# Performance work log

Hardware: AMD Instinct MI355X
Metric: run time of the kernel (lower is better)

## Reference

```python
import jax, jax.numpy as jnp
import numpy as np

E, T, H, I, K = 8, 8192, 1024, 4096, 2  # experts, tokens, hidden, intermediate, top_k


def setup_inputs() -> dict:
    key = jax.random.key(0)
    k1, k2, k3, k4 = jax.random.split(key, 4)
    return {
        "hidden_states": jax.random.normal(k1, (T, H), dtype=jnp.float32),
        "router_weight": jax.random.normal(k2, (E, H), dtype=jnp.float32) * 0.02,
        "gate_up_proj": jax.random.normal(k3, (E, 2 * I, H), dtype=jnp.float32) * 0.02,
        "down_proj": jax.random.normal(k4, (E, H, I), dtype=jnp.float32) * 0.02,
    }


def reference(hidden_states, router_weight, gate_up_proj, down_proj):
    x = hidden_states  # [T, H]
    # --- TopKRouter ---
    router_logits = x @ router_weight.T  # [T, E]
    routing_probs = jax.nn.softmax(router_logits.astype(jnp.float32), axis=-1)
    top_k_weights, top_k_indices = jax.lax.top_k(routing_probs, K)  # [T, K]
    top_k_weights = top_k_weights / jnp.sum(top_k_weights, axis=-1, keepdims=True)  # norm_topk_prob
    top_k_weights = top_k_weights.astype(router_logits.dtype)
    # --- MoEExperts: dense combine weight per (token, expert) ---
    # w_dense[t, e] = sum_k top_k_weights[t, k] * (top_k_indices[t, k] == e)
    tok = jnp.arange(x.shape[0])[:, None]
    w_dense = jnp.zeros((x.shape[0], E), dtype=x.dtype).at[tok, top_k_indices].add(top_k_weights)
    out = jnp.zeros_like(x)
    for e in range(E):  # fixed small expert loop (structurally distinct weights)
        gu = x @ gate_up_proj[e].T          # [T, 2I]
        gate, up = jnp.split(gu, 2, axis=-1)
        y = (jax.nn.silu(gate) * up) @ down_proj[e].T  # [T, H]
        out = out + w_dense[:, e:e + 1] * y
    return out
```

## Files before the change

### kernel.cpp

```cpp
#include <hip/hip_runtime.h>
#include <stdint.h>
#include <math.h>

#define NE 8
#define NT 8192
#define NH 1024
#define NI 4096
#define BM 128
#define BK 32

typedef _Float16 half8 __attribute__((ext_vector_type(8)));
typedef float f32x4 __attribute__((ext_vector_type(4)));

#define OFF_X16   (512u << 10)
#define OFF_ACT   (18u << 20)
#define OFF_GUP16 (146ull << 20)
#define OFF_DP16  (274ull << 20)

__device__ __forceinline__ half8 pack_half8(float4 a, float4 b) {
  half8 h;
  h[0] = (_Float16)a.x; h[1] = (_Float16)a.y; h[2] = (_Float16)a.z; h[3] = (_Float16)a.w;
  h[4] = (_Float16)b.x; h[5] = (_Float16)b.y; h[6] = (_Float16)b.z; h[7] = (_Float16)b.w;
  return h;
}

__device__ __forceinline__ void gload16(const void* g, void* l) {
  __builtin_amdgcn_global_load_lds(
      (const __attribute__((address_space(1))) uint32_t*)g,
      (__attribute__((address_space(3))) uint32_t*)l, 16, 0, 0);
}

#define PIPE_WAIT(N) asm volatile("s_waitcnt vmcnt(" #N ")" ::: "memory")
#define PIPE_BAR() do { asm volatile("" ::: "memory"); \
                        __builtin_amdgcn_s_barrier(); \
                        asm volatile("" ::: "memory"); } while (0)

__global__ __launch_bounds__(256) void convert_w(
    const float* __restrict__ src, _Float16* __restrict__ dst, int n8)
{
  int stride = gridDim.x * 256;
  for (int i = blockIdx.x * 256 + threadIdx.x; i < n8; i += stride) {
    const float4* p = (const float4*)(src + (size_t)i * 8);
    float4 a = p[0], b = p[1];
    *(half8*)(dst + (size_t)i * 8) = pack_half8(a, b);
  }
}

__global__ __launch_bounds__(256) void moe_router(
    const float* __restrict__ x, const float* __restrict__ rw,
    int* __restrict__ iws, _Float16* __restrict__ x16)
{
  int wid  = threadIdx.x >> 6;
  int lane = threadIdx.x & 63;
  int t = (blockIdx.x << 2) + wid;

  const float4* xp4 = (const float4*)(x + (size_t)t * NH + lane * 16);
  float xv[16];
  #pragma unroll
  for (int j = 0; j < 4; ++j) {
    float4 v = xp4[j];
    xv[4*j+0] = v.x; xv[4*j+1] = v.y; xv[4*j+2] = v.z; xv[4*j+3] = v.w;
  }
  half8 h0, h1;
  #pragma unroll
  for (int j = 0; j < 8; ++j) { h0[j] = (_Float16)xv[j]; h1[j] = (_Float16)xv[8+j]; }
  half8* xo = (half8*)(x16 + (size_t)t * NH + lane * 16);
  xo[0] = h0; xo[1] = h1;

  float lg[NE];
  #pragma unroll
  for (int e = 0; e < NE; ++e) {
    const float4* wp4 = (const float4*)(rw + e * NH + lane * 16);
    float s = 0.f;
    #pragma unroll
    for (int j = 0; j < 4; ++j) {
      float4 w = wp4[j];
      s += xv[4*j+0]*w.x + xv[4*j+1]*w.y + xv[4*j+2]*w.z + xv[4*j+3]*w.w;
    }
    lg[e] = s;
  }
  #pragma unroll
  for (int d = 32; d > 0; d >>= 1) {
    #pragma unroll
    for (int e = 0; e < NE; ++e) lg[e] += __shfl_xor(lg[e], d, 64);
  }
  if (lane == 0) {
    int e0 = 0;
    #pragma unroll
    for (int e = 1; e < NE; ++e) if (lg[e] > lg[e0]) e0 = e;
    int e1 = (e0 == 0) ? 1 : 0;
    #pragma unroll
    for (int e = 0; e < NE; ++e) if (e != e0 && lg[e] > lg[e1]) e1 = e;
    float p1 = expf(lg[e1] - lg[e0]);
    float s  = 1.f + p1;
    int*   te = iws + 64;
    float* tw = (float*)(iws + 64 + NT*2);
    te[2*t]   = e0; te[2*t+1] = e1;
    tw[2*t]   = 1.f / s; tw[2*t+1] = p1 / s;
    atomicAdd(iws + e0, 1);
    atomicAdd(iws + e1, 1);
  }
}

__global__ void moe_scan(int* iws) {
  if (threadIdx.x == 0 && blockIdx.x == 0) {
    int* cnt = iws; int* off = iws + 8; int* mbc = iws + 25;
    int o = 0, m = 0;
    for (int e = 0; e < NE; ++e) {
      off[e] = o; mbc[e] = m;
      o += cnt[e]; m += (cnt[e] + BM - 1) / BM;
    }
    off[NE] = o; mbc[NE] = m;
  }
}

__global__ __launch_bounds__(256) void moe_fill(int* __restrict__ iws) {
  int t = blockIdx.x * 256 + threadIdx.x;
  const int*   te = iws + 64;
  const float* tw = (const float*)(iws + 64 + NT*2);
  int*   cursor   = iws + 17;
  const int* off  = iws + 8;
  int*   tok_slot = iws + 64 + NT*4;
  float* w_slot   = (float*)(iws + 64 + NT*6);
  #pragma unroll
  for (int k = 0; k < 2; ++k) {
    int e = te[2*t+k];
    int pos = atomicAdd(&cursor[e], 1);
    int s = off[e] + pos;
    tok_slot[s] = t;
    w_slot[s]   = tw[2*t+k];
  }
}


__global__ __launch_bounds__(256, 2) void moe_gemm1_f16(
    const _Float16* __restrict__ x16, const _Float16* __restrict__ gup16,
    const int* __restrict__ iws, _Float16* __restrict__ act)
{
  const int* cnt = iws; const int* off = iws + 8; const int* mbc = iws + 25;
  const int* tok_slot = iws + 64 + NT*4;
  int bid = blockIdx.x;
  int mb  = bid >> 6;
  int i0  = (bid & 63) << 6;
  if (mb >= mbc[NE]) return;
  int e = 0;
  while (mb >= mbc[e+1]) ++e;
  int mloc  = mb - mbc[e];
  int row0  = off[e] + mloc * BM;
  int nrows = cnt[e] - mloc * BM; if (nrows > BM) nrows = BM;

  __shared__ __align__(16) _Float16 Al [3][BM * BK];
  __shared__ __align__(16) _Float16 Bgl[3][64 * BK];
  __shared__ __align__(16) _Float16 Bul[3][64 * BK];

  int tid = threadIdx.x, wid = tid >> 6, lane = tid & 63;
  int sr0 = wid*16 + (lane >> 2);
  int sr1 = 64 + sr0;
  int slot = lane & 3;
  int ks0 = (slot ^ ((sr0 >> 1) & 3)) * 8;
  int ks1 = (slot ^ ((sr1 >> 1) & 3)) * 8;

  int tok0 = tok_slot[row0 + (sr0 < nrows ? sr0 : 0)];
  int tok1 = tok_slot[row0 + (sr1 < nrows ? sr1 : 0)];
  const _Float16* pA0 = x16 + (size_t)tok0 * NH + ks0;
  const _Float16* pA1 = x16 + (size_t)tok1 * NH + ks1;
  const _Float16* pBg = gup16 + ((size_t)e*2*NI + i0 + sr0) * NH + ks0;
  const _Float16* pBu = pBg + (size_t)NI * NH;

  int wr = (wid >> 1) * 64, wc = (wid & 1) * 32;
  int fr = lane & 15, fq = lane >> 4;

  f32x4 accG[4][2] = {};
  f32x4 accU[4][2] = {};

  _Float16 *A0 = &Al[0][0], *A1 = &Al[1][0], *A2 = &Al[2][0];
  _Float16 *G0 = &Bgl[0][0], *G1 = &Bgl[1][0], *G2 = &Bgl[2][0];
  _Float16 *U0 = &Bul[0][0], *U1 = &Bul[1][0], *U2 = &Bul[2][0];

#define STAGE1(Ab, Gb, Ub, kk) do { \
    gload16(pA0 + (kk), (Ab) + wid*512); \
    gload16(pA1 + (kk), (Ab) + (4+wid)*512); \
    gload16(pBg + (kk), (Gb) + wid*512); \
    gload16(pBu + (kk), (Ub) + wid*512); \
  } while (0)

#define COMPUTE1(Ab, Gb, Ub) do { \
    half8 aF[4]; \
    _Pragma("unroll") \
    for (int m = 0; m < 4; ++m) { \
      int r = wr + m*16 + fr; \
      aF[m] = *(const half8*)((Ab) + r*BK + ((fq ^ ((r>>1)&3)) * 8)); \
    } \
    __builtin_amdgcn_s_setprio(1); \
    _Pragma("unroll") \
    for (int n = 0; n < 2; ++n) { \
      int rb = wc + n*16 + fr; \
      int bo = rb*BK + ((fq ^ ((rb>>1)&3)) * 8); \
      half8 bg = *(const half8*)((Gb) + bo); \
      half8 bu = *(const half8*)((Ub) + bo); \
      _Pragma("unroll") \
      for (int m = 0; m < 4; ++m) \
        accG[m][n] = __builtin_amdgcn_mfma_f32_16x16x32_f16(aF[m], bg, accG[m][n], 0, 0, 0); \
      _Pragma("unroll") \
      for (int m = 0; m < 4; ++m) \
        accU[m][n] = __builtin_amdgcn_mfma_f32_16x16x32_f16(aF[m], bu, accU[m][n], 0, 0, 0); \
    } \
    __builtin_amdgcn_s_setprio(0); \
  } while (0)

#define ROT1() do { _Float16* t_; \
    t_ = A0; A0 = A1; A1 = A2; A2 = t_; \
    t_ = G0; G0 = G1; G1 = G2; G2 = t_; \
    t_ = U0; U0 = U1; U1 = U2; U2 = t_; } while (0)

  STAGE1(A0, G0, U0, 0);
  STAGE1(A1, G1, U1, BK);

  for (int k0 = 0; k0 + 2*BK < NH; k0 += BK) {
    PIPE_WAIT(4);
    PIPE_BAR();
    STAGE1(A2, G2, U2, k0 + 2*BK);
    COMPUTE1(A0, G0, U0);
    ROT1();
  }
  PIPE_WAIT(4);
  PIPE_BAR();
  COMPUTE1(A0, G0, U0);
  ROT1();
  PIPE_WAIT(0);
  PIPE_BAR();
  COMPUTE1(A0, G0, U0);

#undef STAGE1
#undef COMPUTE1
#undef ROT1

  #pragma unroll
  for (int m = 0; m < 4; ++m) {
    #pragma unroll
    for (int j = 0; j < 4; ++j) {
      int rl = wr + m*16 + fq*4 + j;
      if (rl < nrows) {
        _Float16* dst = act + (size_t)(row0 + rl) * NI + i0 + wc + fr;
        #pragma unroll
        for (int n = 0; n < 2; ++n) {
          float g = accG[m][n][j], u = accU[m][n][j];
          float a = (g / (1.f + __expf(-g))) * u;
          dst[n*16] = (_Float16)a;
        }
      }
    }
  }
}

__global__ __launch_bounds__(256, 4) void moe_gemm2_f16(
    const _Float16* __restrict__ act, const _Float16* __restrict__ dp16,
    const int* __restrict__ iws, float* __restrict__ out)
{
  const int* cnt = iws; const int* off = iws + 8; const int* mbc = iws + 25;
  const int* tok_slot = iws + 64 + NT*4;
  const float* w_slot = (const float*)(iws + 64 + NT*6);
  int bid = blockIdx.x;
  int mb  = bid >> 4;
  int h0  = (bid & 15) << 6;
  if (mb >= mbc[NE]) return;
  int e = 0;
  while (mb >= mbc[e+1]) ++e;
  int mloc  = mb - mbc[e];
  int row0  = off[e] + mloc * BM;
  int nrows = cnt[e] - mloc * BM; if (nrows > BM) nrows = BM;

  __shared__ __align__(16) _Float16 Al[3][BM * BK];
  __shared__ __align__(16) _Float16 Bl[3][64 * BK];

  int tid = threadIdx.x, wid = tid >> 6, lane = tid & 63;
  int sr0 = wid*16 + (lane >> 2);
  int sr1 = 64 + sr0;
  int slot = lane & 3;
  int ks0 = (slot ^ ((sr0 >> 1) & 3)) * 8;
  int ks1 = (slot ^ ((sr1 >> 1) & 3)) * 8;

  const _Float16* pA0 = act + (size_t)(row0 + (sr0 < nrows ? sr0 : 0)) * NI + ks0;
  const _Float16* pA1 = act + (size_t)(row0 + (sr1 < nrows ? sr1 : 0)) * NI + ks1;
  const _Float16* pB  = dp16 + ((size_t)e*NH + h0 + sr0) * NI + ks0;

  int wr = (wid >> 1) * 64, wc = (wid & 1) * 32;
  int fr = lane & 15, fq = lane >> 4;

  f32x4 acc[4][2] = {};

  _Float16 *A0 = &Al[0][0], *A1 = &Al[1][0], *A2 = &Al[2][0];
  _Float16 *B0 = &Bl[0][0], *B1 = &Bl[1][0], *B2 = &Bl[2][0];

#define STAGE2(Ab, Bb, kk) do { \
    gload16(pA0 + (kk), (Ab) + wid*512); \
    gload16(pA1 + (kk), (Ab) + (4+wid)*512); \
    gload16(pB  + (kk), (Bb) + wid*512); \
  } while (0)

#define COMPUTE2(Ab, Bb) do { \
    half8 aF[4]; \
    _Pragma("unroll") \
    for (int m = 0; m < 4; ++m) { \
      int r = wr + m*16 + fr; \
      aF[m] = *(const half8*)((Ab) + r*BK + ((fq ^ ((r>>1)&3)) * 8)); \
    } \
    __builtin_amdgcn_s_setprio(1); \
    _Pragma("unroll") \
    for (int n = 0; n < 2; ++n) { \
      int rb = wc + n*16 + fr; \
      half8 b = *(const half8*)((Bb) + rb*BK + ((fq ^ ((rb>>1)&3)) * 8)); \
      _Pragma("unroll") \
      for (int m = 0; m < 4; ++m) \
        acc[m][n] = __builtin_amdgcn_mfma_f32_16x16x32_f16(aF[m], b, acc[m][n], 0, 0, 0); \
    } \
    __builtin_amdgcn_s_setprio(0); \
  } while (0)

#define ROT2() do { _Float16* t_; \
    t_ = A0; A0 = A1; A1 = A2; A2 = t_; \
    t_ = B0; B0 = B1; B1 = B2; B2 = t_; } while (0)

  STAGE2(A0, B0, 0);
  STAGE2(A1, B1, BK);

  for (int k0 = 0; k0 + 2*BK < NI; k0 += BK) {
    PIPE_WAIT(3);
    PIPE_BAR();
    STAGE2(A2, B2, k0 + 2*BK);
    COMPUTE2(A0, B0);
    ROT2();
  }
  PIPE_WAIT(3);
  PIPE_BAR();
  COMPUTE2(A0, B0);
  ROT2();
  PIPE_WAIT(0);
  PIPE_BAR();
  COMPUTE2(A0, B0);

#undef STAGE2
#undef COMPUTE2
#undef ROT2

  #pragma unroll
  for (int m = 0; m < 4; ++m) {
    #pragma unroll
    for (int j = 0; j < 4; ++j) {
      int rl = wr + m*16 + fq*4 + j;
      if (rl < nrows) {
        int slotr = row0 + rl;
        float wgt = w_slot[slotr];
        int tok   = tok_slot[slotr];
        float* dst = out + (size_t)tok * NH + h0 + wc + fr;
        #pragma unroll
        for (int n = 0; n < 2; ++n)
          atomicAdd(dst + n*16, acc[m][n][j] * wgt);
      }
    }
  }
}

extern "C" void kernel_launch(void* const* d_in, const int* in_sizes, int n_in,
                              void* d_out, int out_size, void* d_ws, size_t ws_size,
                              hipStream_t stream) {
  const float* x   = (const float*)d_in[0];
  const float* rw  = (const float*)d_in[1];
  const float* gup = (const float*)d_in[2];
  const float* dp  = (const float*)d_in[3];
  float* out = (float*)d_out;
  int* iws = (int*)d_ws;
  _Float16* x16   = (_Float16*)((char*)d_ws + OFF_X16);
  _Float16* act   = (_Float16*)((char*)d_ws + OFF_ACT);
  _Float16* gup16 = (_Float16*)((char*)d_ws + OFF_GUP16);
  _Float16* dp16  = (_Float16*)((char*)d_ws + OFF_DP16);

  hipMemsetAsync(d_out, 0, (size_t)NT * NH * sizeof(float), stream);
  hipMemsetAsync(d_ws, 0, 512, stream);

  convert_w<<<2048, 256, 0, stream>>>(gup, gup16, NE*2*NI*NH/8);
  convert_w<<<2048, 256, 0, stream>>>(dp,  dp16,  NE*NH*NI/8);

  moe_router<<<NT / 4, 256, 0, stream>>>(x, rw, iws, x16);
  moe_scan<<<1, 64, 0, stream>>>(iws);
  moe_fill<<<NT / 256, 256, 0, stream>>>(iws);

  int nmb = NT * 2 / BM + NE;
  moe_gemm1_f16<<<nmb * (NI / 64), 256, 0, stream>>>(x16, gup16, iws, act);
  moe_gemm2_f16<<<nmb * (NH / 64), 256, 0, stream>>>(act, dp16, iws, out);
}
```

Baseline: 1.058 ms.

## Restructure gate/up GEMM into 8-wave 128x128 tiles with interleaved load/MFMA phases

The first expert GEMM moves from 256-thread blocks with 128x64 tiles and BK=32 to 512-thread blocks with 128x128 output tiles and BK=64. A is double-buffered and gate/up weights are triple-buffered in LDS. Each K step is split into four barrier-separated MFMA phases, with global-to-LDS loads issued between them and an XOR swizzle over 8 chunks, so memory traffic overlaps compute and weight reuse per block goes up. In exchange it uses much more LDS (occupancy of one block per CU), adds many barriers, and makes the pipeline wait-count logic more fragile.

```diff
diff --git a/kernel.cpp b/kernel.cpp
--- a/kernel.cpp
+++ b/kernel.cpp
@@ -34,6 +34,9 @@
 #define PIPE_BAR() do { asm volatile("" ::: "memory"); \
                         __builtin_amdgcn_s_barrier(); \
                         asm volatile("" ::: "memory"); } while (0)
+#define LGKM0() do { asm volatile("s_waitcnt lgkmcnt(0)" ::: "memory"); \
+                     __builtin_amdgcn_sched_barrier(0); } while (0)
+#define MF(a,b,c) __builtin_amdgcn_mfma_f32_16x16x32_f16((a),(b),(c),0,0,0)
 
 __global__ __launch_bounds__(256) void convert_w(
     const float* __restrict__ src, _Float16* __restrict__ dst, int n8)
@@ -132,16 +135,15 @@
   }
 }
 
-
-__global__ __launch_bounds__(256, 2) void moe_gemm1_f16(
+__global__ __launch_bounds__(512, 1) void moe_gemm1_f16(
     const _Float16* __restrict__ x16, const _Float16* __restrict__ gup16,
     const int* __restrict__ iws, _Float16* __restrict__ act)
 {
   const int* cnt = iws; const int* off = iws + 8; const int* mbc = iws + 25;
   const int* tok_slot = iws + 64 + NT*4;
   int bid = blockIdx.x;
-  int mb  = bid >> 6;
-  int i0  = (bid & 63) << 6;
+  int mb  = bid >> 5;
+  int i0  = (bid & 31) << 7;
   if (mb >= mbc[NE]) return;
   int e = 0;
   while (mb >= mbc[e+1]) ++e;
@@ -149,91 +151,134 @@
   int row0  = off[e] + mloc * BM;
   int nrows = cnt[e] - mloc * BM; if (nrows > BM) nrows = BM;
 
-  __shared__ __align__(16) _Float16 Al [3][BM * BK];
-  __shared__ __align__(16) _Float16 Bgl[3][64 * BK];
-  __shared__ __align__(16) _Float16 Bul[3][64 * BK];
+  __shared__ __align__(16) _Float16 Asb[2][128*64];
+  __shared__ __align__(16) _Float16 Gsb[3][128*64];
+  __shared__ __align__(16) _Float16 Usb[3][128*64];
 
   int tid = threadIdx.x, wid = tid >> 6, lane = tid & 63;
-  int sr0 = wid*16 + (lane >> 2);
-  int sr1 = 64 + sr0;
-  int slot = lane & 3;
-  int ks0 = (slot ^ ((sr0 >> 1) & 3)) * 8;
-  int ks1 = (slot ^ ((sr1 >> 1) & 3)) * 8;
-
-  int tok0 = tok_slot[row0 + (sr0 < nrows ? sr0 : 0)];
-  int tok1 = tok_slot[row0 + (sr1 < nrows ? sr1 : 0)];
-  const _Float16* pA0 = x16 + (size_t)tok0 * NH + ks0;
-  const _Float16* pA1 = x16 + (size_t)tok1 * NH + ks1;
-  const _Float16* pBg = gup16 + ((size_t)e*2*NI + i0 + sr0) * NH + ks0;
-  const _Float16* pBu = pBg + (size_t)NI * NH;
-
-  int wr = (wid >> 1) * 64, wc = (wid & 1) * 32;
+  int srow = (wid << 3) + (lane >> 3);
+  int ss8  = ((lane & 7) ^ (srow & 7)) << 3;
+  int r1   = srow + 64;
+  int tokA0 = tok_slot[row0 + (srow < nrows ? srow : 0)];
+  int tokA1 = tok_slot[row0 + (r1   < nrows ? r1   : 0)];
+  const _Float16* pA0 = x16 + (size_t)tokA0 * NH + ss8;
+  const _Float16* pA1 = x16 + (size_t)tokA1 * NH + ss8;
+  const _Float16* pG0 = gup16 + ((size_t)e*2*NI + i0 + srow) * NH + ss8;
+  const _Float16* pG1 = pG0 + (size_t)64 * NH;
+  const _Float16* pU0 = pG0 + (size_t)NI * NH;
+  const _Float16* pU1 = pG1 + (size_t)NI * NH;
+  int ldst = wid << 9;
+
+  int wr = (wid >> 2) * 64, wc = (wid & 3) * 32;
   int fr = lane & 15, fq = lane >> 4;
 
   f32x4 accG[4][2] = {};
   f32x4 accU[4][2] = {};
 
-  _Float16 *A0 = &Al[0][0], *A1 = &Al[1][0], *A2 = &Al[2][0];
-  _Float16 *G0 = &Bgl[0][0], *G1 = &Bgl[1][0], *G2 = &Bgl[2][0];
-  _Float16 *U0 = &Bul[0][0], *U1 = &Bul[1][0], *U2 = &Bul[2][0];
-
-#define STAGE1(Ab, Gb, Ub, kk) do { \
-    gload16(pA0 + (kk), (Ab) + wid*512); \
-    gload16(pA1 + (kk), (Ab) + (4+wid)*512); \
-    gload16(pBg + (kk), (Gb) + wid*512); \
-    gload16(pBu + (kk), (Ub) + wid*512); \
-  } while (0)
-
-#define COMPUTE1(Ab, Gb, Ub) do { \
-    half8 aF[4]; \
-    _Pragma("unroll") \
-    for (int m = 0; m < 4; ++m) { \
-      int r = wr + m*16 + fr; \
-      aF[m] = *(const half8*)((Ab) + r*BK + ((fq ^ ((r>>1)&3)) * 8)); \
-    } \
-    __builtin_amdgcn_s_setprio(1); \
-    _Pragma("unroll") \
-    for (int n = 0; n < 2; ++n) { \
-      int rb = wc + n*16 + fr; \
-      int bo = rb*BK + ((fq ^ ((rb>>1)&3)) * 8); \
-      half8 bg = *(const half8*)((Gb) + bo); \
-      half8 bu = *(const half8*)((Ub) + bo); \
-      _Pragma("unroll") \
-      for (int m = 0; m < 4; ++m) \
-        accG[m][n] = __builtin_amdgcn_mfma_f32_16x16x32_f16(aF[m], bg, accG[m][n], 0, 0, 0); \
-      _Pragma("unroll") \
-      for (int m = 0; m < 4; ++m) \
-        accU[m][n] = __builtin_amdgcn_mfma_f32_16x16x32_f16(aF[m], bu, accU[m][n], 0, 0, 0); \
-    } \
-    __builtin_amdgcn_s_setprio(0); \
-  } while (0)
+  _Float16 *Aa = Asb[0], *Ab = Asb[1];
+  _Float16 *G0b = Gsb[0], *G1b = Gsb[1], *G2b = Gsb[2];
+  _Float16 *U0b = Usb[0], *U1b = Usb[1], *U2b = Usb[2];
+
+#define SA0(B,kk) gload16(pA0 + (kk), (B) + ldst)
+#define SA1(B,kk) gload16(pA1 + (kk), (B) + 4096 + ldst)
+#define SG0(B,kk) gload16(pG0 + (kk), (B) + ldst)
+#define SG1(B,kk) gload16(pG1 + (kk), (B) + 4096 + ldst)
+#define SU0(B,kk) gload16(pU0 + (kk), (B) + ldst)
+#define SU1(B,kk) gload16(pU1 + (kk), (B) + 4096 + ldst)
+#define LDT(B,r,k) (*(const half8*)((B) + (size_t)(r)*64 + ((((k)*4+fq) ^ ((r)&7)) << 3)))
+
+#define TILE1(Ac,Gc,Uc, S0,S1,S2,S3,S4,S5) do { \
+   \
+  half8 aa00=LDT(Ac,wr+fr,0),    aa01=LDT(Ac,wr+fr,1); \
+  half8 aa10=LDT(Ac,wr+16+fr,0), aa11=LDT(Ac,wr+16+fr,1); \
+  half8 g00=LDT(Gc,wc+fr,0),     g01=LDT(Gc,wc+fr,1); \
+  half8 g10=LDT(Gc,wc+16+fr,0),  g11=LDT(Gc,wc+16+fr,1); \
+  S0; \
+  PIPE_BAR(); LGKM0(); \
+  __builtin_amdgcn_s_setprio(1); \
+  accG[0][0]=MF(aa00,g00,accG[0][0]); accG[0][0]=MF(aa01,g01,accG[0][0]); \
+  accG[0][1]=MF(aa00,g10,accG[0][1]); accG[0][1]=MF(aa01,g11,accG[0][1]); \
+  accG[1][0]=MF(aa10,g00,accG[1][0]); accG[1][0]=MF(aa11,g01,accG[1][0]); \
+  accG[1][1]=MF(aa10,g10,accG[1][1]); accG[1][1]=MF(aa11,g11,accG[1][1]); \
+  __builtin_amdgcn_s_setprio(0); \
+  PIPE_BAR(); \
+   \
+  half8 u00=LDT(Uc,wc+fr,0),     u01=LDT(Uc,wc+fr,1); \
+  half8 u10=LDT(Uc,wc+16+fr,0),  u11=LDT(Uc,wc+16+fr,1); \
+  S1; S2; \
+  PIPE_BAR(); LGKM0(); \
+  __builtin_amdgcn_s_setprio(1); \
+  accU[0][0]=MF(aa00,u00,accU[0][0]); accU[0][0]=MF(aa01,u01,accU[0][0]); \
+  accU[0][1]=MF(aa00,u10,accU[0][1]); accU[0][1]=MF(aa01,u11,accU[0][1]); \
+  accU[1][0]=MF(aa10,u00,accU[1][0]); accU[1][0]=MF(aa11,u01,accU[1][0]); \
+  accU[1][1]=MF(aa10,u10,accU[1][1]); accU[1][1]=MF(aa11,u11,accU[1][1]); \
+  __builtin_amdgcn_s_setprio(0); \
+  PIPE_BAR(); \
+   \
+  half8 ab00=LDT(Ac,wr+32+fr,0), ab01=LDT(Ac,wr+32+fr,1); \
+  half8 ab10=LDT(Ac,wr+48+fr,0), ab11=LDT(Ac,wr+48+fr,1); \
+  S3; S4; \
+  PIPE_BAR(); LGKM0(); \
+  __builtin_amdgcn_s_setprio(1); \
+  accG[2][0]=MF(ab00,g00,accG[2][0]); accG[2][0]=MF(ab01,g01,accG[2][0]); \
+  accG[2][1]=MF(ab00,g10,accG[2][1]); accG[2][1]=MF(ab01,g11,accG[2][1]); \
+  accG[3][0]=MF(ab10,g00,accG[3][0]); accG[3][0]=MF(ab11,g01,accG[3][0]); \
+  accG[3][1]=MF(ab10,g10,accG[3][1]); accG[3][1]=MF(ab11,g11,accG[3][1]); \
+  __builtin_amdgcn_s_setprio(0); \
+  PIPE_BAR(); \
+   \
+  S5; \
+  PIPE_BAR(); \
+  __builtin_amdgcn_s_setprio(1); \
+  accU[2][0]=MF(ab00,u00,accU[2][0]); accU[2][0]=MF(ab01,u01,accU[2][0]); \
+  accU[2][1]=MF(ab00,u10,accU[2][1]); accU[2][1]=MF(ab01,u11,accU[2][1]); \
+  accU[3][0]=MF(ab10,u00,accU[3][0]); accU[3][0]=MF(ab11,u01,accU[3][0]); \
+  accU[3][1]=MF(ab10,u10,accU[3][1]); accU[3][1]=MF(ab11,u11,accU[3][1]); \
+  __builtin_amdgcn_s_setprio(0); \
+  PIPE_BAR(); \
+} while (0)
 
 #define ROT1() do { _Float16* t_; \
-    t_ = A0; A0 = A1; A1 = A2; A2 = t_; \
-    t_ = G0; G0 = G1; G1 = G2; G2 = t_; \
-    t_ = U0; U0 = U1; U1 = U2; U2 = t_; } while (0)
-
-  STAGE1(A0, G0, U0, 0);
-  STAGE1(A1, G1, U1, BK);
-
-  for (int k0 = 0; k0 + 2*BK < NH; k0 += BK) {
+    t_ = Aa;  Aa  = Ab;  Ab  = t_; \
+    t_ = G0b; G0b = G1b; G1b = G2b; G2b = t_; \
+    t_ = U0b; U0b = U1b; U1b = U2b; U2b = t_; } while (0)
+
+  SG0(G0b, 0);  SG1(G0b, 0);  SU0(U0b, 0);  SU1(U0b, 0);
+  SA0(Aa, 0);   SA1(Aa, 0);
+  SG0(G1b, 64); SG1(G1b, 64); SU0(U1b, 64); SU1(U1b, 64);
+
+  for (int t = 0; t < 14; ++t) {
     PIPE_WAIT(4);
     PIPE_BAR();
-    STAGE1(A2, G2, U2, k0 + 2*BK);
-    COMPUTE1(A0, G0, U0);
+    int kA = (t + 1) << 6, kG = (t + 2) << 6;
+    TILE1(Aa, G0b, U0b,
+          SA0(Ab, kA), SA1(Ab, kA),
+          SG0(G2b, kG), SG1(G2b, kG),
+          SU0(U2b, kG), SU1(U2b, kG));
     ROT1();
   }
-  PIPE_WAIT(4);
-  PIPE_BAR();
-  COMPUTE1(A0, G0, U0);
-  ROT1();
+  {
+    PIPE_WAIT(4);
+    PIPE_BAR();
+    int kA = 15 << 6;
+    TILE1(Aa, G0b, U0b,
+          SA0(Ab, kA), SA1(Ab, kA),
+          (void)0, (void)0, (void)0, (void)0);
+    ROT1();
+  }
   PIPE_WAIT(0);
   PIPE_BAR();
-  COMPUTE1(A0, G0, U0);
-
-#undef STAGE1
-#undef COMPUTE1
+  TILE1(Aa, G0b, U0b, (void)0, (void)0, (void)0, (void)0, (void)0, (void)0);
+
+#undef TILE1
 #undef ROT1
+#undef SA0
+#undef SA1
+#undef SG0
+#undef SG1
+#undef SU0
+#undef SU1
+#undef LDT
 
   #pragma unroll
   for (int m = 0; m < 4; ++m) {
@@ -386,6 +431,6 @@
   moe_fill<<<NT / 256, 256, 0, stream>>>(iws);
 
   int nmb = NT * 2 / BM + NE;
-  moe_gemm1_f16<<<nmb * (NI / 64), 256, 0, stream>>>(x16, gup16, iws, act);
+  moe_gemm1_f16<<<nmb * (NI / 128), 512, 0, stream>>>(x16, gup16, iws, act);
   moe_gemm2_f16<<<nmb * (NH / 64), 256, 0, stream>>>(act, dp16, iws, out);
 }
```

Result: slower. 1.089 ms (+2.8%).
